# Optimization experiments

Hardware: AMD Instinct MI355X
Metric: run time of the kernel (lower is better)

Reference implementation:

```python
import jax, jax.numpy as jnp
import numpy as np

NUM_USERS = 100000
NUM_RECIPES = 200000
EMB = 32
RDIM = 96
D = EMB + RDIM  # 128, shared node feature dim
E = 1500000
NUM_LAYERS = 3


def setup_inputs() -> dict:
    key = jax.random.key(0)
    k1, k2, k3, k4, k5, k6 = jax.random.split(key, 6)
    usr_emb = 0.1 * jax.random.normal(k1, (NUM_USERS, D), jnp.float32)      # usr_embedding.weight (init std=0.1)
    rcp_emb = 0.1 * jax.random.normal(k2, (NUM_RECIPES, EMB), jnp.float32)  # rcp_embedding.weight
    recipe_feat = jax.random.normal(k3, (NUM_RECIPES, RDIM), jnp.float32)   # x_dict['recipe']
    user_idx = jax.random.randint(k4, (E,), 0, NUM_USERS, jnp.int32)        # edge_index row 0 (user)
    rcp_idx = jax.random.randint(k5, (E,), 0, NUM_RECIPES, jnp.int32)       # edge_index row 1 (recipe)
    edge_weight = 1.0 + 4.0 * jax.random.uniform(k6, (E,), jnp.float32)     # review scores in [1,5]
    return {"usr_emb": usr_emb, "rcp_emb": rcp_emb, "recipe_feat": recipe_feat,
            "edge_weight": edge_weight, "user_idx": user_idx, "rcp_idx": rcp_idx}


def reference(usr_emb, rcp_emb, recipe_feat, edge_weight, user_idx, rcp_idx):
    seg = jax.ops.segment_sum
    alpha = 1.0 / (NUM_LAYERS + 1)

    # LightGCN symmetric normalization with review-score edge weights
    # (HeteroLGConv: msg = x_src[src] * w / sqrt(deg_w(src) * deg_w(dst)); sum-aggregate at dst).
    deg_u = seg(edge_weight, user_idx, num_segments=NUM_USERS)    # weighted user degree
    deg_r = seg(edge_weight, rcp_idx, num_segments=NUM_RECIPES)   # weighted recipe degree
    norm = edge_weight * jax.lax.rsqrt(jnp.clip(deg_u[user_idx] * deg_r[rcp_idx], 1e-12, None))  # [E]

    rcp_x = jnp.concatenate([rcp_emb, recipe_feat], axis=1)  # [R, D]
    usr_x = usr_emb                                           # [U, D]
    rec_out = rcp_x * alpha
    usr_out = usr_x * alpha

    for _ in range(NUM_LAYERS):
        # user -> recipe propagation
        rcp_x = seg(usr_x[user_idx] * norm[:, None], rcp_idx, num_segments=NUM_RECIPES)
        rec_out = rec_out + rcp_x * alpha
        # recipe -> user propagation (reverse edges)
        usr_x = seg(rcp_x[rcp_idx] * norm[:, None], user_idx, num_segments=NUM_USERS)
        usr_out = usr_out + usr_x * alpha

    return usr_out, rec_out
```

## Files before the change

kernel.cpp:

```cpp
#include <hip/hip_runtime.h>
#include <hip/hip_fp16.h>


typedef unsigned long long ull;

constexpr int NU   = 100000;
constexpr int NR   = 200000;
constexpr int EMB  = 32;
constexpr int RDIM = 96;
constexpr int D    = 128;
constexpr int NE   = 1500000;
constexpr float ALPHA = 0.25f;

constexpr ull DEG_MASK = (1ULL << 44) - 1;
constexpr float DEG_SCALE = 1048576.0f;
constexpr float DEG_INV   = 1.0f / 1048576.0f;

constexpr int QB = (NE / 4 + 255) / 256;
constexpr int CB = (NU * D / 16 + 255) / 256;


__device__ __forceinline__ unsigned pack_bf16x2(float x, float y) {
    unsigned ux = __float_as_uint(x);
    unsigned uy = __float_as_uint(y);
    ux += 0x7fffu + ((ux >> 16) & 1u);
    uy += 0x7fffu + ((uy >> 16) & 1u);
    return (ux >> 16) | (uy & 0xffff0000u);
}

__device__ __forceinline__ float blo(unsigned u) { return __uint_as_float(u << 16); }
__device__ __forceinline__ float bhi(unsigned u) { return __uint_as_float(u & 0xffff0000u); }


__global__ void deg_bf16_kernel(const float4* __restrict__ w4,
                                const int4* __restrict__ u4,
                                const int4* __restrict__ r4,
                                ull* __restrict__ pk_u,
                                ull* __restrict__ pk_r,
                                ull* __restrict__ rankp,
                                const float4* __restrict__ usr_emb4,
                                uint4* __restrict__ emb_h4) {
    if ((int)blockIdx.x >= QB) {
        int t = ((int)blockIdx.x - QB) * 256 + threadIdx.x;
        int base = t * 4;
        float4 a = usr_emb4[base], b = usr_emb4[base + 1];
        float4 c = usr_emb4[base + 2], d = usr_emb4[base + 3];
        uint4 o0 = {pack_bf16x2(a.x, a.y), pack_bf16x2(a.z, a.w),
                    pack_bf16x2(b.x, b.y), pack_bf16x2(b.z, b.w)};
        uint4 o1 = {pack_bf16x2(c.x, c.y), pack_bf16x2(c.z, c.w),
                    pack_bf16x2(d.x, d.y), pack_bf16x2(d.z, d.w)};
        emb_h4[t * 2]     = o0;
        emb_h4[t * 2 + 1] = o1;
        return;
    }
    int i = blockIdx.x * blockDim.x + threadIdx.x;
    if (i < NE / 4) {
        float4 wv = w4[i];
        int4 uu = u4[i];
        int4 rr = r4[i];
        ull v0 = (1ULL << 44) | (ull)(wv.x * DEG_SCALE + 0.5f);
        ull v1 = (1ULL << 44) | (ull)(wv.y * DEG_SCALE + 0.5f);
        ull v2 = (1ULL << 44) | (ull)(wv.z * DEG_SCALE + 0.5f);
        ull v3 = (1ULL << 44) | (ull)(wv.w * DEG_SCALE + 0.5f);
        ull ou0 = atomicAdd(&pk_u[uu.x], v0);
        ull or0 = atomicAdd(&pk_r[rr.x], v0);
        ull ou1 = atomicAdd(&pk_u[uu.y], v1);
        ull or1 = atomicAdd(&pk_r[rr.y], v1);
        ull ou2 = atomicAdd(&pk_u[uu.z], v2);
        ull or2 = atomicAdd(&pk_r[rr.z], v2);
        ull ou3 = atomicAdd(&pk_u[uu.w], v3);
        ull or3 = atomicAdd(&pk_r[rr.w], v3);
        ull pk = ((ou0 >> 44) & 0xFF)         | (((or0 >> 44) & 0xFF) << 8)
               | (((ou1 >> 44) & 0xFF) << 16) | (((or1 >> 44) & 0xFF) << 24)
               | (((ou2 >> 44) & 0xFF) << 32) | (((or2 >> 44) & 0xFF) << 40)
               | (((ou3 >> 44) & 0xFF) << 48) | (((or3 >> 44) & 0xFF) << 56);
        rankp[i] = pk;
    }
}


__global__ void scan_block_both(const ull* __restrict__ pk_r,
                                const ull* __restrict__ pk_u,
                                int* __restrict__ rp_r,
                                int* __restrict__ rp_u,
                                int* __restrict__ bsum, int nbR) {
    __shared__ int tmp[256];
    bool isR = (int)blockIdx.x < nbR;
    const ull* pk = isR ? pk_r : pk_u;
    int* excl = isR ? rp_r : rp_u;
    int ncnt  = isR ? NR : NU;
    int b     = isR ? (int)blockIdx.x : (int)blockIdx.x - nbR;
    int nscan = ncnt + 1;
    int i = b * 256 + threadIdx.x;
    int v = 0;
    if (i < ncnt) v = ((int)(pk[i] >> 44) + 7) & ~7;
    tmp[threadIdx.x] = v;
    __syncthreads();
    for (int off = 1; off < 256; off <<= 1) {
        int t = (threadIdx.x >= off) ? tmp[threadIdx.x - off] : 0;
        __syncthreads();
        tmp[threadIdx.x] += t;
        __syncthreads();
    }
    if (i < nscan) excl[i] = tmp[threadIdx.x] - v;
    if (threadIdx.x == 255) bsum[blockIdx.x] = tmp[255];
}

__global__ void scan_bsum2(int* __restrict__ bsum, int nbR, int nbU) {
    __shared__ int tmp[1024];
    int off = (blockIdx.x == 0) ? 0 : nbR;
    int nb  = (blockIdx.x == 0) ? nbR : nbU;
    int i = threadIdx.x;
    int v = (i < nb) ? bsum[off + i] : 0;
    tmp[i] = v;
    __syncthreads();
    for (int o = 1; o < 1024; o <<= 1) {
        int t = (i >= o) ? tmp[i - o] : 0;
        __syncthreads();
        tmp[i] += t;
        __syncthreads();
    }
    if (i < nb) bsum[off + i] = tmp[i] - v;
}

__global__ void finalize_both(const int* __restrict__ rp_r,
                              const int* __restrict__ rp_u,
                              const ull* __restrict__ pk_r,
                              const ull* __restrict__ pk_u,
                              int2* __restrict__ combo_r,
                              int2* __restrict__ combo_u,
                              const int* __restrict__ bsum, int nbR) {
    bool isR = (int)blockIdx.x < nbR;
    const int* rp = isR ? rp_r : rp_u;
    const ull* pk = isR ? pk_r : pk_u;
    int2* combo   = isR ? combo_r : combo_u;
    int ncnt  = isR ? NR : NU;
    int b     = isR ? (int)blockIdx.x : (int)blockIdx.x - nbR;
    int i = b * 256 + threadIdx.x;
    if (i < ncnt + 1) {
        int rpv = rp[i] + bsum[blockIdx.x];
        float deg = (i < ncnt) ? (float)(pk[i] & DEG_MASK) * DEG_INV : 0.0f;
        combo[i] = make_int2(rpv, __float_as_int(deg));
    }
}


__global__ void fill_kernel(const float4* __restrict__ w4,
                            const int4* __restrict__ u4,
                            const int4* __restrict__ r4,
                            const int2* __restrict__ combo_u,
                            const int2* __restrict__ combo_r,
                            const ull* __restrict__ rankp,
                            unsigned* __restrict__ pair_u,
                            unsigned* __restrict__ pair_r) {
    int i = blockIdx.x * blockDim.x + threadIdx.x;
    if (i >= NE / 4) return;
    float4 wv = w4[i];
    int4 uu = u4[i];
    int4 rr = r4[i];
    ull rk = rankp[i];

#define FILL_ONE(WW, U, R, SH)                                               \
    {                                                                        \
        int2 cu = combo_u[(U)];                                              \
        int2 cr = combo_r[(R)];                                              \
        float du = __int_as_float(cu.y);                                     \
        float dr = __int_as_float(cr.y);                                     \
        float nv = (WW) * rsqrtf(fmaxf(du * dr, 1e-12f));                    \
        unsigned short hb = __half_as_ushort(__float2half(nv));              \
        unsigned n14 = ((unsigned)hb + 1u) >> 1;                             \
        int rku = (int)((rk >> (SH)) & 0xFF);                                \
        int rkr = (int)((rk >> ((SH) + 8)) & 0xFF);                          \
        pair_r[cr.x + rkr] = (n14 << 18) | (unsigned)(U);                    \
        pair_u[cu.x + rku] = (n14 << 18) | (unsigned)(R);                    \
    }

    FILL_ONE(wv.x, uu.x, rr.x, 0)
    FILL_ONE(wv.y, uu.y, rr.y, 16)
    FILL_ONE(wv.z, uu.z, rr.z, 32)
    FILL_ONE(wv.w, uu.w, rr.w, 48)
#undef FILL_ONE
}

__global__ void gather_rows(const unsigned* __restrict__ src,
                            const int2* __restrict__ combo,
                            const unsigned* __restrict__ pair,
                            unsigned* __restrict__ xout,
                            float* __restrict__ out_f,
                            const unsigned* __restrict__ prev1,
                            const unsigned* __restrict__ prev2,
                            const float* __restrict__ init_a,
                            const float* __restrict__ init_b,
                            int nrows) {
    int wid  = (blockIdx.x * blockDim.x + threadIdx.x) >> 6;
    wid = __builtin_amdgcn_readfirstlane(wid);
    int lane = threadIdx.x & 63;
    if (wid >= nrows) return;

    int beg = __builtin_amdgcn_readfirstlane(combo[wid].x);
    int end = __builtin_amdgcn_readfirstlane(combo[wid + 1].x);
    float x0 = 0.f, y0 = 0.f, x1 = 0.f, y1 = 0.f;
    float x2 = 0.f, y2 = 0.f, x3 = 0.f, y3 = 0.f;

#define LOAD_EDGE(P, AX, AY)                                                  \
    {                                                                         \
        unsigned s = (P) & 0x3FFFFu;                                          \
        float n = __half2float(__ushort_as_half(                              \
                      (unsigned short)(((P) >> 18) << 1)));                   \
        unsigned v = src[(size_t)s * 64 + lane];                              \
        AX += n * __uint_as_float(v << 16);                                   \
        AY += n * __uint_as_float(v & 0xffff0000u);                           \
    }

    int e = beg;
    for (; e + 16 <= end; e += 16) {
        uint4 pa = *reinterpret_cast<const uint4*>(pair + e);
        uint4 pb = *reinterpret_cast<const uint4*>(pair + e + 4);
        uint4 pc = *reinterpret_cast<const uint4*>(pair + e + 8);
        uint4 pd = *reinterpret_cast<const uint4*>(pair + e + 12);
        LOAD_EDGE(pa.x, x0, y0) LOAD_EDGE(pa.y, x1, y1)
        LOAD_EDGE(pa.z, x2, y2) LOAD_EDGE(pa.w, x3, y3)
        LOAD_EDGE(pb.x, x0, y0) LOAD_EDGE(pb.y, x1, y1)
        LOAD_EDGE(pb.z, x2, y2) LOAD_EDGE(pb.w, x3, y3)
        LOAD_EDGE(pc.x, x0, y0) LOAD_EDGE(pc.y, x1, y1)
        LOAD_EDGE(pc.z, x2, y2) LOAD_EDGE(pc.w, x3, y3)
        LOAD_EDGE(pd.x, x0, y0) LOAD_EDGE(pd.y, x1, y1)
        LOAD_EDGE(pd.z, x2, y2) LOAD_EDGE(pd.w, x3, y3)
    }
    for (; e < end; e += 8) {
        uint4 pa = *reinterpret_cast<const uint4*>(pair + e);
        uint4 pb = *reinterpret_cast<const uint4*>(pair + e + 4);
        LOAD_EDGE(pa.x, x0, y0) LOAD_EDGE(pa.y, x1, y1)
        LOAD_EDGE(pa.z, x2, y2) LOAD_EDGE(pa.w, x3, y3)
        LOAD_EDGE(pb.x, x0, y0) LOAD_EDGE(pb.y, x1, y1)
        LOAD_EDGE(pb.z, x2, y2) LOAD_EDGE(pb.w, x3, y3)
    }
#undef LOAD_EDGE

    x0 = (x0 + x1) + (x2 + x3);
    y0 = (y0 + y1) + (y2 + y3);

    size_t xo = (size_t)wid * 64 + lane;
    if (xout) xout[xo] = pack_bf16x2(x0, y0);

    if (out_f) {
        size_t o = (size_t)wid * D + lane * 2;
        float2 b;
        if (init_b) {
            b = (lane < 16)
                ? *reinterpret_cast<const float2*>(init_a + (size_t)wid * EMB + lane * 2)
                : *reinterpret_cast<const float2*>(init_b + (size_t)wid * RDIM + (lane * 2 - EMB));
        } else {
            b = *reinterpret_cast<const float2*>(init_a + o);
        }
        if (prev1) {
            unsigned v1 = prev1[xo], v2 = prev2[xo];
            float lo = b.x + blo(v1) + blo(v2) + x0;
            float hi = b.y + bhi(v1) + bhi(v2) + y0;
            float2 ov = {ALPHA * lo, ALPHA * hi};
            *reinterpret_cast<float2*>(out_f + o) = ov;
        } else {
            float2 ov = {ALPHA * (b.x + x0), ALPHA * (b.y + y0)};
            *reinterpret_cast<float2*>(out_f + o) = ov;
        }
    }
}

__global__ void gather_rows_acc(const unsigned* __restrict__ src,
                                const int2* __restrict__ combo,
                                const unsigned* __restrict__ pair,
                                unsigned* __restrict__ xout,
                                float* __restrict__ out_f,
                                int nrows) {
    int wid  = (blockIdx.x * blockDim.x + threadIdx.x) >> 6;
    wid = __builtin_amdgcn_readfirstlane(wid);
    int lane = threadIdx.x & 63;
    if (wid >= nrows) return;
    int beg = __builtin_amdgcn_readfirstlane(combo[wid].x);
    int end = __builtin_amdgcn_readfirstlane(combo[wid + 1].x);
    float x0 = 0.f, y0 = 0.f;
    for (int e = beg; e < end; ++e) {
        unsigned P = pair[e];
        unsigned s = P & 0x3FFFFu;
        float n = __half2float(__ushort_as_half((unsigned short)((P >> 18) << 1)));
        unsigned v = src[(size_t)s * 64 + lane];
        x0 += n * blo(v); y0 += n * bhi(v);
    }
    size_t xo = (size_t)wid * 64 + lane;
    if (xout) xout[xo] = pack_bf16x2(x0, y0);
    size_t o = (size_t)wid * D + lane * 2;
    float2 ov = *reinterpret_cast<float2*>(out_f + o);
    ov.x += ALPHA * x0; ov.y += ALPHA * y0;
    *reinterpret_cast<float2*>(out_f + o) = ov;
}

__global__ void init_out_kernel(const float* __restrict__ usr_emb,
                                const float* __restrict__ rcp_emb,
                                const float* __restrict__ rfeat,
                                float* __restrict__ out) {
    long long i = blockIdx.x * (long long)blockDim.x + threadIdx.x;
    const long long UD = (long long)NU * D;
    const long long RD = (long long)NR * D;
    if (i < UD) {
        out[i] = ALPHA * usr_emb[i];
    } else if (i < UD + RD) {
        long long j = i - UD;
        int r = (int)(j >> 7);
        int d = (int)(j & 127);
        float v = (d < EMB) ? rcp_emb[(long long)r * EMB + d]
                            : rfeat[(long long)r * RDIM + (d - EMB)];
        out[i] = ALPHA * v;
    }
}


extern "C" void kernel_launch(void* const* d_in, const int* in_sizes, int n_in,
                              void* d_out, int out_size, void* d_ws, size_t ws_size,
                              hipStream_t stream) {
    const float* usr_emb = (const float*)d_in[0];
    const float* rcp_emb = (const float*)d_in[1];
    const float* rfeat   = (const float*)d_in[2];
    const float* w       = (const float*)d_in[3];
    const int*   ui      = (const int*)d_in[4];
    const int*   ri      = (const int*)d_in[5];

    float* out     = (float*)d_out;
    float* usr_out = out;
    float* rec_out = out + (size_t)NU * D;

    char* p0 = (char*)d_ws;
    char* p = p0;
    auto take = [&](size_t bytes) -> char* {
        char* q = p;
        p += (bytes + 255) & ~(size_t)255;
        return q;
    };

    const int PR_SLOTS = NE + 7 * NR + 16;
    const int PU_SLOTS = NE + 7 * NU + 16;

    ull*      pk_u   = (ull*)take((size_t)NU * 8);
    ull*      pk_r   = (ull*)take((size_t)NR * 8);
    unsigned* pair_r = (unsigned*)take((size_t)PR_SLOTS * 4);
    unsigned* pair_u = (unsigned*)take((size_t)PU_SLOTS * 4);
    char*     zero_end = p;
    ull*      rankp   = (ull*)take((size_t)(NE / 4) * 8);
    int*      rp_r    = (int*)take((size_t)(NR + 1) * 4);
    int*      rp_u    = (int*)take((size_t)(NU + 1) * 4);
    int2*     combo_r = (int2*)take((size_t)(NR + 1) * 8);
    int2*     combo_u = (int2*)take((size_t)(NU + 1) * 8);
    int*      bsum    = (int*)take(4096 * 4);
    unsigned* emb_h   = (unsigned*)take((size_t)NU * 64 * 4);

    const size_t xr_b = (size_t)NR * 64 * 4;
    const size_t xu_b = (size_t)NU * 64 * 4;
    size_t used_head = (size_t)(p - p0);
    bool deferred = (ws_size >= used_head + 3 * ((xr_b + 255) & ~(size_t)255)
                                         + 2 * ((xu_b + 255) & ~(size_t)255));

    unsigned *xr0, *xr1, *xr2, *xu0, *xu1;
    if (deferred) {
        xr0 = (unsigned*)take(xr_b); xr1 = (unsigned*)take(xr_b); xr2 = (unsigned*)take(xr_b);
        xu0 = (unsigned*)take(xu_b); xu1 = (unsigned*)take(xu_b);
    } else {
        xr0 = xr1 = xr2 = (unsigned*)take(xr_b);
        xu0 = xu1 = (unsigned*)take(xu_b);
    }

    const int B = 256;

    hipMemsetAsync(pk_u, 0, (size_t)(zero_end - (char*)pk_u), stream);

    deg_bf16_kernel<<<QB + CB, B, 0, stream>>>(
        (const float4*)w, (const int4*)ui, (const int4*)ri,
        pk_u, pk_r, rankp, (const float4*)usr_emb, (uint4*)emb_h);

    const int nbR = (NR + 1 + 255) / 256;
    const int nbU = (NU + 1 + 255) / 256;
    scan_block_both<<<nbR + nbU, 256, 0, stream>>>(pk_r, pk_u, rp_r, rp_u, bsum, nbR);
    scan_bsum2<<<2, 1024, 0, stream>>>(bsum, nbR, nbU);
    finalize_both<<<nbR + nbU, 256, 0, stream>>>(rp_r, rp_u, pk_r, pk_u,
                                                 combo_r, combo_u, bsum, nbR);

    fill_kernel<<<QB, B, 0, stream>>>((const float4*)w, (const int4*)ui,
                                      (const int4*)ri, combo_u, combo_r,
                                      rankp, pair_u, pair_r);

    const int GB_R = (NR * 64 + B - 1) / B;
    const int GB_U = (NU * 64 + B - 1) / B;

    if (deferred) {
        gather_rows<<<GB_R, B, 0, stream>>>(emb_h, combo_r, pair_r, xr0,
                                            nullptr, nullptr, nullptr, nullptr, nullptr, NR);
        gather_rows<<<GB_U, B, 0, stream>>>(xr0, combo_u, pair_u, xu0,
                                            nullptr, nullptr, nullptr, nullptr, nullptr, NU);
        gather_rows<<<GB_R, B, 0, stream>>>(xu0, combo_r, pair_r, xr1,
                                            nullptr, nullptr, nullptr, nullptr, nullptr, NR);
        gather_rows<<<GB_U, B, 0, stream>>>(xr1, combo_u, pair_u, xu1,
                                            nullptr, nullptr, nullptr, nullptr, nullptr, NU);
        gather_rows<<<GB_R, B, 0, stream>>>(xu1, combo_r, pair_r, xr2,
                                            rec_out, xr0, xr1, rcp_emb, rfeat, NR);
        gather_rows<<<GB_U, B, 0, stream>>>(xr2, combo_u, pair_u, nullptr,
                                            usr_out, xu0, xu1, usr_emb, nullptr, NU);
    } else {
        long long tot = (long long)(NU + NR) * D;
        init_out_kernel<<<(int)((tot + B - 1) / B), B, 0, stream>>>(usr_emb, rcp_emb, rfeat, out);
        gather_rows_acc<<<GB_R, B, 0, stream>>>(emb_h, combo_r, pair_r, xr0, rec_out, NR);
        gather_rows_acc<<<GB_U, B, 0, stream>>>(xr0, combo_u, pair_u, xu0, usr_out, NU);
        gather_rows_acc<<<GB_R, B, 0, stream>>>(xu0, combo_r, pair_r, xr0, rec_out, NR);
        gather_rows_acc<<<GB_U, B, 0, stream>>>(xr0, combo_u, pair_u, xu0, usr_out, NU);
        gather_rows_acc<<<GB_R, B, 0, stream>>>(xu0, combo_r, pair_r, xr0, rec_out, NR);
        gather_rows_acc<<<GB_U, B, 0, stream>>>(xr0, combo_u, pair_u, nullptr, usr_out, NU);
    }
}
```

Measured before the change: 614.4 us.

## Replace global atomic CSR build with two-level bucketed counting sort

Replaces the global 64-bit atomic degree/rank pass and random-scatter fill with a bucketed pipeline. It builds a per-block histogram over coarse node buckets, scans it, and scatters packed edge records into buckets. Degrees and final CSR slots are then computed with shared-memory atomics inside each bucket. This targets contended global atomics and scattered writes, at the cost of more kernel launches, an extra pass over edge records, and reusing feature buffers as scratch. Weights are now rounded to fp16 before the degree sum, which slightly changes degree precision.

```diff
diff --git a/kernel.cpp b/kernel.cpp
--- a/kernel.cpp
+++ b/kernel.cpp
@@ -16,8 +16,12 @@
 constexpr float DEG_SCALE = 1048576.0f;
 constexpr float DEG_INV   = 1.0f / 1048576.0f;
 
-constexpr int QB = (NE / 4 + 255) / 256;
-constexpr int CB = (NU * D / 16 + 255) / 256;
+constexpr int NBK    = 391;
+constexpr int SPAN_R = 512;
+constexpr int SPAN_U = 256;
+constexpr int EPB    = 4096;
+constexpr int B1     = (NE + EPB - 1) / EPB;
+constexpr int CB     = (NU * D / 16 + 255) / 256;
 
 
 __device__ __forceinline__ unsigned pack_bf16x2(float x, float y) {
@@ -32,49 +36,150 @@
 __device__ __forceinline__ float bhi(unsigned u) { return __uint_as_float(u & 0xffff0000u); }
 
 
-__global__ void deg_bf16_kernel(const float4* __restrict__ w4,
-                                const int4* __restrict__ u4,
-                                const int4* __restrict__ r4,
-                                ull* __restrict__ pk_u,
-                                ull* __restrict__ pk_r,
-                                ull* __restrict__ rankp,
-                                const float4* __restrict__ usr_emb4,
-                                uint4* __restrict__ emb_h4) {
-    if ((int)blockIdx.x >= QB) {
-        int t = ((int)blockIdx.x - QB) * 256 + threadIdx.x;
-        int base = t * 4;
-        float4 a = usr_emb4[base], b = usr_emb4[base + 1];
-        float4 c = usr_emb4[base + 2], d = usr_emb4[base + 3];
-        uint4 o0 = {pack_bf16x2(a.x, a.y), pack_bf16x2(a.z, a.w),
-                    pack_bf16x2(b.x, b.y), pack_bf16x2(b.z, b.w)};
-        uint4 o1 = {pack_bf16x2(c.x, c.y), pack_bf16x2(c.z, c.w),
-                    pack_bf16x2(d.x, d.y), pack_bf16x2(d.z, d.w)};
-        emb_h4[t * 2]     = o0;
-        emb_h4[t * 2 + 1] = o1;
+__global__ void hist_kernel(const int* __restrict__ ui,
+                            const int* __restrict__ ri,
+                            unsigned* __restrict__ hist_u,
+                            unsigned* __restrict__ hist_r,
+                            const float4* __restrict__ usr_emb4,
+                            uint4* __restrict__ emb_h4) {
+    if ((int)blockIdx.x >= B1) {
+        int t = ((int)blockIdx.x - B1) * 256 + threadIdx.x;
+        if (t < NU * D / 16) {
+            int base = t * 4;
+            float4 a = usr_emb4[base], b = usr_emb4[base + 1];
+            float4 c = usr_emb4[base + 2], d = usr_emb4[base + 3];
+            uint4 o0 = {pack_bf16x2(a.x, a.y), pack_bf16x2(a.z, a.w),
+                        pack_bf16x2(b.x, b.y), pack_bf16x2(b.z, b.w)};
+            uint4 o1 = {pack_bf16x2(c.x, c.y), pack_bf16x2(c.z, c.w),
+                        pack_bf16x2(d.x, d.y), pack_bf16x2(d.z, d.w)};
+            emb_h4[t * 2]     = o0;
+            emb_h4[t * 2 + 1] = o1;
+        }
         return;
     }
-    int i = blockIdx.x * blockDim.x + threadIdx.x;
-    if (i < NE / 4) {
-        float4 wv = w4[i];
-        int4 uu = u4[i];
-        int4 rr = r4[i];
-        ull v0 = (1ULL << 44) | (ull)(wv.x * DEG_SCALE + 0.5f);
-        ull v1 = (1ULL << 44) | (ull)(wv.y * DEG_SCALE + 0.5f);
-        ull v2 = (1ULL << 44) | (ull)(wv.z * DEG_SCALE + 0.5f);
-        ull v3 = (1ULL << 44) | (ull)(wv.w * DEG_SCALE + 0.5f);
-        ull ou0 = atomicAdd(&pk_u[uu.x], v0);
-        ull or0 = atomicAdd(&pk_r[rr.x], v0);
-        ull ou1 = atomicAdd(&pk_u[uu.y], v1);
-        ull or1 = atomicAdd(&pk_r[rr.y], v1);
-        ull ou2 = atomicAdd(&pk_u[uu.z], v2);
-        ull or2 = atomicAdd(&pk_r[rr.z], v2);
-        ull ou3 = atomicAdd(&pk_u[uu.w], v3);
-        ull or3 = atomicAdd(&pk_r[rr.w], v3);
-        ull pk = ((ou0 >> 44) & 0xFF)         | (((or0 >> 44) & 0xFF) << 8)
-               | (((ou1 >> 44) & 0xFF) << 16) | (((or1 >> 44) & 0xFF) << 24)
-               | (((ou2 >> 44) & 0xFF) << 32) | (((or2 >> 44) & 0xFF) << 40)
-               | (((ou3 >> 44) & 0xFF) << 48) | (((or3 >> 44) & 0xFF) << 56);
-        rankp[i] = pk;
+    __shared__ unsigned hu[NBK], hr[NBK];
+    for (int j = threadIdx.x; j < NBK; j += 256) { hu[j] = 0; hr[j] = 0; }
+    __syncthreads();
+    int base = blockIdx.x * EPB;
+    for (int k = 0; k < 16; ++k) {
+        int i = base + k * 256 + threadIdx.x;
+        if (i < NE) {
+            atomicAdd(&hu[ui[i] >> 8], 1u);
+            atomicAdd(&hr[ri[i] >> 9], 1u);
+        }
+    }
+    __syncthreads();
+    for (int j = threadIdx.x; j < NBK; j += 256) {
+        hist_u[j * B1 + blockIdx.x] = hu[j];
+        hist_r[j * B1 + blockIdx.x] = hr[j];
+    }
+}
+
+
+__global__ void scan_hist(unsigned* __restrict__ hist_r,
+                          unsigned* __restrict__ hist_u,
+                          unsigned* __restrict__ btot) {
+    __shared__ unsigned tmp[512];
+    bool isR = (int)blockIdx.x < NBK;
+    int j = isR ? (int)blockIdx.x : (int)blockIdx.x - NBK;
+    unsigned* h = (isR ? hist_r : hist_u) + (size_t)j * B1;
+    int i = threadIdx.x;
+    unsigned v = (i < B1) ? h[i] : 0;
+    tmp[i] = v;
+    __syncthreads();
+    for (int o = 1; o < 512; o <<= 1) {
+        unsigned t = (i >= o) ? tmp[i - o] : 0;
+        __syncthreads();
+        tmp[i] += t;
+        __syncthreads();
+    }
+    if (i < B1) h[i] = tmp[i] - v;
+    if (i == 511) btot[blockIdx.x] = tmp[511];
+}
+
+
+__global__ void scan_btot(const unsigned* __restrict__ btot,
+                          unsigned* __restrict__ boff_r,
+                          unsigned* __restrict__ boff_u) {
+    __shared__ unsigned tmp[512];
+    bool isR = (blockIdx.x == 0);
+    unsigned* boff = isR ? boff_r : boff_u;
+    int i = threadIdx.x;
+    unsigned v = (i < NBK) ? btot[(isR ? 0 : NBK) + i] : 0;
+    tmp[i] = v;
+    __syncthreads();
+    for (int o = 1; o < 512; o <<= 1) {
+        unsigned t = (i >= o) ? tmp[i - o] : 0;
+        __syncthreads();
+        tmp[i] += t;
+        __syncthreads();
+    }
+    if (i < NBK) boff[i] = tmp[i] - v;
+    if (i == 0) boff[NBK] = tmp[511];
+}
+
+
+__global__ void scatter_kernel(const int* __restrict__ ui,
+                               const int* __restrict__ ri,
+                               const float* __restrict__ w,
+                               const unsigned* __restrict__ hist_u,
+                               const unsigned* __restrict__ hist_r,
+                               const unsigned* __restrict__ boff_u,
+                               const unsigned* __restrict__ boff_r,
+                               ull* __restrict__ buf_u,
+                               ull* __restrict__ buf_r) {
+    __shared__ unsigned cu[NBK], cr[NBK];
+    for (int j = threadIdx.x; j < NBK; j += 256) {
+        cu[j] = boff_u[j] + hist_u[j * B1 + blockIdx.x];
+        cr[j] = boff_r[j] + hist_r[j * B1 + blockIdx.x];
+    }
+    __syncthreads();
+    int base = blockIdx.x * EPB;
+    for (int k = 0; k < 16; ++k) {
+        int i = base + k * 256 + threadIdx.x;
+        if (i < NE) {
+            int u = ui[i], r = ri[i];
+            ull wh = (ull)__half_as_ushort(__float2half(w[i]));
+            ull rec_r = (ull)(unsigned)u | ((ull)(r & 511) << 18) | (wh << 32);
+            ull rec_u = (ull)(unsigned)r | ((ull)(u & 255) << 18) | (wh << 32);
+            unsigned sr = atomicAdd(&cr[r >> 9], 1u);
+            unsigned su = atomicAdd(&cu[u >> 8], 1u);
+            buf_r[sr] = rec_r;
+            buf_u[su] = rec_u;
+        }
+    }
+}
+
+
+__global__ void count_kernel(const ull* __restrict__ buf_r,
+                             const ull* __restrict__ buf_u,
+                             const unsigned* __restrict__ boff_r,
+                             const unsigned* __restrict__ boff_u,
+                             ull* __restrict__ pk_r,
+                             ull* __restrict__ pk_u) {
+    bool isR = (int)blockIdx.x < NBK;
+    int j = isR ? (int)blockIdx.x : (int)blockIdx.x - NBK;
+    const ull* buf = isR ? buf_r : buf_u;
+    const unsigned* boff = isR ? boff_r : boff_u;
+    ull* pk = isR ? pk_r : pk_u;
+    int span = isR ? SPAN_R : SPAN_U;
+    int nnode = isR ? NR : NU;
+    __shared__ unsigned cnt[512], wfx[512];
+    for (int i = threadIdx.x; i < span; i += 256) { cnt[i] = 0; wfx[i] = 0; }
+    __syncthreads();
+    unsigned beg = boff[j], end = boff[j + 1];
+    for (unsigned e = beg + threadIdx.x; e < end; e += 256) {
+        ull rec = buf[e];
+        int dlow = (int)((rec >> 18) & 511);
+        float wv = __half2float(__ushort_as_half((unsigned short)(rec >> 32)));
+        atomicAdd(&cnt[dlow], 1u);
+        atomicAdd(&wfx[dlow], (unsigned)(wv * DEG_SCALE + 0.5f));
+    }
+    __syncthreads();
+    int nb = j * span;
+    for (int i = threadIdx.x; i < span; i += 256) {
+        int node = nb + i;
+        if (node < nnode) pk[node] = ((ull)cnt[i] << 44) | (ull)wfx[i];
     }
 }
 
@@ -145,42 +250,50 @@
 }
 
 
-__global__ void fill_kernel(const float4* __restrict__ w4,
-                            const int4* __restrict__ u4,
-                            const int4* __restrict__ r4,
+__global__ void emit_kernel(const ull* __restrict__ buf_r,
+                            const ull* __restrict__ buf_u,
+                            const unsigned* __restrict__ boff_r,
+                            const unsigned* __restrict__ boff_u,
+                            const int2* __restrict__ combo_r,
                             const int2* __restrict__ combo_u,
-                            const int2* __restrict__ combo_r,
-                            const ull* __restrict__ rankp,
-                            unsigned* __restrict__ pair_u,
-                            unsigned* __restrict__ pair_r) {
-    int i = blockIdx.x * blockDim.x + threadIdx.x;
-    if (i >= NE / 4) return;
-    float4 wv = w4[i];
-    int4 uu = u4[i];
-    int4 rr = r4[i];
-    ull rk = rankp[i];
-
-#define FILL_ONE(WW, U, R, SH)                                               \
-    {                                                                        \
-        int2 cu = combo_u[(U)];                                              \
-        int2 cr = combo_r[(R)];                                              \
-        float du = __int_as_float(cu.y);                                     \
-        float dr = __int_as_float(cr.y);                                     \
-        float nv = (WW) * rsqrtf(fmaxf(du * dr, 1e-12f));                    \
-        unsigned short hb = __half_as_ushort(__float2half(nv));              \
-        unsigned n14 = ((unsigned)hb + 1u) >> 1;                             \
-        int rku = (int)((rk >> (SH)) & 0xFF);                                \
-        int rkr = (int)((rk >> ((SH) + 8)) & 0xFF);                          \
-        pair_r[cr.x + rkr] = (n14 << 18) | (unsigned)(U);                    \
-        pair_u[cu.x + rku] = (n14 << 18) | (unsigned)(R);                    \
-    }
-
-    FILL_ONE(wv.x, uu.x, rr.x, 0)
-    FILL_ONE(wv.y, uu.y, rr.y, 16)
-    FILL_ONE(wv.z, uu.z, rr.z, 32)
-    FILL_ONE(wv.w, uu.w, rr.w, 48)
-#undef FILL_ONE
-}
+                            unsigned* __restrict__ pair_r,
+                            unsigned* __restrict__ pair_u) {
+    bool isR = (int)blockIdx.x < NBK;
+    int j = isR ? (int)blockIdx.x : (int)blockIdx.x - NBK;
+    const ull* buf = isR ? buf_r : buf_u;
+    const unsigned* boff = isR ? boff_r : boff_u;
+    const int2* combo  = isR ? combo_r : combo_u;
+    const int2* comboO = isR ? combo_u : combo_r;
+    unsigned* pair = isR ? pair_r : pair_u;
+    int span = isR ? SPAN_R : SPAN_U;
+    int nnode = isR ? NR : NU;
+    __shared__ int rp_l[512];
+    __shared__ float deg_l[512];
+    __shared__ unsigned cur[512];
+    int nb = j * span;
+    for (int i = threadIdx.x; i < span; i += 256) {
+        int node = nb + i;
+        int2 c = (node < nnode) ? combo[node] : make_int2(0, 0);
+        rp_l[i] = c.x;
+        deg_l[i] = __int_as_float(c.y);
+        cur[i] = 0;
+    }
+    __syncthreads();
+    unsigned beg = boff[j], end = boff[j + 1];
+    for (unsigned e = beg + threadIdx.x; e < end; e += 256) {
+        ull rec = buf[e];
+        unsigned src = (unsigned)(rec & 0x3FFFFu);
+        int dlow = (int)((rec >> 18) & 511);
+        float wv = __half2float(__ushort_as_half((unsigned short)(rec >> 32)));
+        float dO = __int_as_float(comboO[src].y);
+        float nv = wv * rsqrtf(fmaxf(deg_l[dlow] * dO, 1e-12f));
+        unsigned short hb = __half_as_ushort(__float2half(nv));
+        unsigned n14 = ((unsigned)hb + 1u) >> 1;
+        unsigned rank = atomicAdd(&cur[dlow], 1u);
+        pair[rp_l[dlow] + (int)rank] = (n14 << 18) | src;
+    }
+}
+
 
 __global__ void gather_rows(const unsigned* __restrict__ src,
                             const int2* __restrict__ combo,
@@ -339,17 +452,19 @@
     const int PR_SLOTS = NE + 7 * NR + 16;
     const int PU_SLOTS = NE + 7 * NU + 16;
 
-    ull*      pk_u   = (ull*)take((size_t)NU * 8);
-    ull*      pk_r   = (ull*)take((size_t)NR * 8);
     unsigned* pair_r = (unsigned*)take((size_t)PR_SLOTS * 4);
     unsigned* pair_u = (unsigned*)take((size_t)PU_SLOTS * 4);
     char*     zero_end = p;
-    ull*      rankp   = (ull*)take((size_t)(NE / 4) * 8);
+    ull*      pk_u    = (ull*)take((size_t)NU * 8);
+    ull*      pk_r    = (ull*)take((size_t)NR * 8);
     int*      rp_r    = (int*)take((size_t)(NR + 1) * 4);
     int*      rp_u    = (int*)take((size_t)(NU + 1) * 4);
     int2*     combo_r = (int2*)take((size_t)(NR + 1) * 8);
     int2*     combo_u = (int2*)take((size_t)(NU + 1) * 8);
     int*      bsum    = (int*)take(4096 * 4);
+    unsigned* btot    = (unsigned*)take((size_t)2 * NBK * 4);
+    unsigned* boff_r  = (unsigned*)take((size_t)(NBK + 1) * 4);
+    unsigned* boff_u  = (unsigned*)take((size_t)(NBK + 1) * 4);
     unsigned* emb_h   = (unsigned*)take((size_t)NU * 64 * 4);
 
     const size_t xr_b = (size_t)NR * 64 * 4;
@@ -367,13 +482,22 @@
         xu0 = xu1 = (unsigned*)take(xu_b);
     }
 
+    ull*      buf_r  = (ull*)xr0;
+    ull*      buf_u  = buf_r + NE;
+    unsigned* hist_r = (unsigned*)(buf_u + NE);
+    unsigned* hist_u = hist_r + (size_t)NBK * B1;
+
     const int B = 256;
 
-    hipMemsetAsync(pk_u, 0, (size_t)(zero_end - (char*)pk_u), stream);
-
-    deg_bf16_kernel<<<QB + CB, B, 0, stream>>>(
-        (const float4*)w, (const int4*)ui, (const int4*)ri,
-        pk_u, pk_r, rankp, (const float4*)usr_emb, (uint4*)emb_h);
+    hipMemsetAsync(pair_r, 0, (size_t)(zero_end - (char*)pair_r), stream);
+
+    hist_kernel<<<B1 + CB, B, 0, stream>>>(ui, ri, hist_u, hist_r,
+                                           (const float4*)usr_emb, (uint4*)emb_h);
+    scan_hist<<<2 * NBK, 512, 0, stream>>>(hist_r, hist_u, btot);
+    scan_btot<<<2, 512, 0, stream>>>(btot, boff_r, boff_u);
+    scatter_kernel<<<B1, B, 0, stream>>>(ui, ri, w, hist_u, hist_r,
+                                         boff_u, boff_r, buf_u, buf_r);
+    count_kernel<<<2 * NBK, B, 0, stream>>>(buf_r, buf_u, boff_r, boff_u, pk_r, pk_u);
 
     const int nbR = (NR + 1 + 255) / 256;
     const int nbU = (NU + 1 + 255) / 256;
@@ -381,10 +505,8 @@
     scan_bsum2<<<2, 1024, 0, stream>>>(bsum, nbR, nbU);
     finalize_both<<<nbR + nbU, 256, 0, stream>>>(rp_r, rp_u, pk_r, pk_u,
                                                  combo_r, combo_u, bsum, nbR);
-
-    fill_kernel<<<QB, B, 0, stream>>>((const float4*)w, (const int4*)ui,
-                                      (const int4*)ri, combo_u, combo_r,
-                                      rankp, pair_u, pair_r);
+    emit_kernel<<<2 * NBK, B, 0, stream>>>(buf_r, buf_u, boff_r, boff_u,
+                                           combo_r, combo_u, pair_r, pair_u);
 
     const int GB_R = (NR * 64 + B - 1) / B;
     const int GB_U = (NU * 64 + B - 1) / B;
```

Measured after the change: 558.0 us. 9.2% less time.
